# Performance work log

Hardware: AMD Instinct MI355X
Metric: run time of the kernel (lower is better)

Reference implementation:

```python
import jax, jax.numpy as jnp
import numpy as np

L = 2000          # number of residues (sequence length)
FEATURES_L = 2048 # config.features_L pad target
W = 7             # config.window_size
D = 54            # per-residue feature dim after bert_lin
H = 3             # attention heads
HD = D // H       # head dim = 18
CH = 32           # conv hidden channels
KS = (3, 5, 7)    # config.kernels


def setup_inputs() -> dict:
    key = jax.random.key(0)
    ks = jax.random.split(key, 20)
    n = lambda k, s, sc=0.02: jax.random.normal(k, s, jnp.float32) * sc
    return {
        'beft_f': jax.random.normal(ks[0], (L, 1024), jnp.float32),
        'pssm_f': jax.random.normal(ks[1], (L, 20), jnp.float32),
        'hmm_f': jax.random.normal(ks[2], (L, 30), jnp.float32),
        'dssp_f': jax.random.normal(ks[3], (L, 14), jnp.float32),
        'W_bert': n(ks[4], (1024, D)), 'b_bert': jnp.zeros((D,), jnp.float32),
        'ln_g1': jnp.ones((D,), jnp.float32), 'ln_b1': jnp.zeros((D,), jnp.float32),
        'ln_g2': jnp.ones((D,), jnp.float32), 'ln_b2': jnp.zeros((D,), jnp.float32),
        'conv1_w': n(ks[5], (CH, 1, 3, 1), 0.1), 'conv1_b': n(ks[6], (CH,), 0.1),
        'prelu_a': jnp.array(0.25, jnp.float32),
        'conv2_w': n(ks[7], (CH, 1, 5, 1), 0.1), 'conv2_b': n(ks[8], (CH,), 0.1),
        'conv3_w': n(ks[9], (CH, 1, 7, 1), 0.1), 'conv3_b': n(ks[10], (CH,), 0.1),
        'W1': n(ks[11], (972, 256)), 'b1': jnp.zeros((256,), jnp.float32),
        'W2': n(ks[12], (CH * 256, 256)), 'b2': jnp.zeros((256,), jnp.float32),
    }


def _ln(x, g, b, eps=1e-5):
    m = x.mean(-1, keepdims=True)
    v = ((x - m) ** 2).mean(-1, keepdims=True)
    return (x - m) * jax.lax.rsqrt(v + eps) * g + b


def _attn(x, g, b):
    # x: (L, W, D); no qkv projections, no 1/sqrt(d) scaling (as in source)
    qh = x.reshape(x.shape[0], W, H, HD)
    s = jnp.einsum('bqhd,bkhd->bhqk', qh, qh)
    p = jax.nn.softmax(s, axis=-1)
    o = jnp.einsum('bhqk,bkhd->bqhd', p, qh).reshape(x.shape[0], W, D)
    return _ln(o, g, b)


def _conv_branch(x, w, bias, k, act):
    pad = (k - 1) // 2
    c = jax.lax.conv_general_dilated(x, w, (1, 1), ((pad, pad), (0, 0)),
                                     dimension_numbers=('NCHW', 'OIHW', 'NCHW'))
    c = act(c + bias[None, :, None, None])
    c = jax.lax.reduce_window(c, -jnp.inf, jax.lax.max,
                              (1, 1, k, 1), (1, 1, 1, 1), 'VALID')
    return c.reshape(c.shape[0], CH, -1)  # (FEATURES_L, 32, (W-k+1)*2D)


def _forward(beft_f, W_bert, b_bert, ln_g1, ln_b1, ln_g2, ln_b2,
             conv1_w, conv1_b, prelu_a, conv2_w, conv2_b, conv3_w, conv3_b,
             W1, b1, W2, b2):
    f = beft_f @ W_bert + b_bert  # (L, 54)
    # sliding-window gather replicating the source python loop exactly:
    # interior rows i in (W, L-W): window = f[i-4 : i+3]; boundary rows: [f[i], 0...0]
    i = jnp.arange(L)
    j = jnp.arange(W)
    gidx = jnp.clip(i[:, None] - (W // 2 + 1) + j[None, :], 0, L - 1)
    win_int = f[gidx]                                   # (L, 7, 54)
    win_bnd = jnp.zeros((L, W, D), f.dtype).at[:, 0].set(f)
    boundary = (i <= W) | (i + W >= L)
    new_f = jnp.where(boundary[:, None, None], win_bnd, win_int)
    sf = _attn(new_f, ln_g1, ln_b1)
    sf = _attn(sf, ln_g2, ln_b2)
    cat = jnp.concatenate([new_f, sf], axis=2)          # (L, 7, 108)
    x = jnp.pad(cat, ((0, FEATURES_L - L), (0, 0), (0, 0)))[:, None]  # (FL,1,7,108)
    prelu = lambda z: jnp.where(z >= 0, z, prelu_a * z)
    feats = jnp.concatenate([
        _conv_branch(x, conv1_w, conv1_b, KS[0], prelu),
        _conv_branch(x, conv2_w, conv2_b, KS[1], jax.nn.relu),
        _conv_branch(x, conv3_w, conv3_b, KS[2], jax.nn.relu)], axis=2)  # (FL,32,972)
    y = feats[:L] @ W1 + b1                             # (L, 32, 256)
    y = y.reshape(L, CH * 256) @ W2 + b2                # (L, 256)
    return jnp.where(y >= 0, y, 0.01 * y)               # leaky_relu


def reference(beft_f, pssm_f, hmm_f, dssp_f, W_bert, b_bert, ln_g1, ln_b1,
              ln_g2, ln_b2, conv1_w, conv1_b, prelu_a, conv2_w, conv2_b,
              conv3_w, conv3_b, W1, b1, W2, b2):
    # pssm_f / hmm_f / dssp_f are accepted but unused in the source forward
    return _forward(beft_f, W_bert, b_bert, ln_g1, ln_b1, ln_g2, ln_b2,
                    conv1_w, conv1_b, prelu_a, conv2_w, conv2_b,
                    conv3_w, conv3_b, W1, b1, W2, b2)
```

## Files before the change

kernel.cpp:

```cpp
#include <hip/hip_runtime.h>

#define L_RES 2000
#define DF 54
#define WIN 7

typedef short bf16x8 __attribute__((ext_vector_type(8)));
typedef float f32x4 __attribute__((ext_vector_type(4)));
typedef unsigned short ushort8v __attribute__((ext_vector_type(8)));

__device__ __forceinline__ unsigned short f2bf(float f) {
    unsigned int u = __float_as_uint(f);
    unsigned int r = (u + 0x7FFFu + ((u >> 16) & 1u)) >> 16;
    return (unsigned short)r;
}
__device__ __forceinline__ float bf2f(unsigned short h) {
    return __uint_as_float(((unsigned int)h) << 16);
}
__device__ __forceinline__ void gload16(const unsigned short* g, unsigned short* l) {
    __builtin_amdgcn_global_load_lds(
        (const __attribute__((address_space(1))) void*)g,
        (__attribute__((address_space(3))) void*)l, 16, 0, 0);
}

__global__ __launch_bounds__(256) void prep_w(const float* __restrict__ Wb,
                                              unsigned short* __restrict__ B2T,
                                              const float* __restrict__ W1,
                                              unsigned short* __restrict__ P) {
    int bid = blockIdx.x;
    if (bid < 768) {
        int idx = bid * 256 + threadIdx.x;
        int n = idx / 3072, col = idx % 3072;
        int seg = col >> 10, k = col & 1023;
        unsigned short r = 0;
        if (n < DF) {
            float v = Wb[(size_t)k * DF + n];
            unsigned short hi = f2bf(v);
            r = (seg < 2) ? hi : f2bf(v - bf2f(hi));
        }
        B2T[idx] = r;
    } else {
        int idx = (bid - 768) * 256 + threadIdx.x;
        int e = idx & 7, l = (idx >> 3) & 63, g = (idx >> 9) & 31, nb = idx >> 14;
        int ks = g >> 1, kk = g & 1;
        int n = nb * 16 + (l & 15);
        int k = ks * 64 + kk * 32 + (l >> 4) * 8 + e;
        P[idx] = (k < 972) ? f2bf(W1[(size_t)k * 256 + n]) : (unsigned short)0;
    }
}

__global__ __launch_bounds__(256) void bert_mfma(const float* __restrict__ beft,
                                                 const unsigned short* __restrict__ B2T,
                                                 float* __restrict__ bpart) {
    __shared__ unsigned short ldsA[128 * 64];
    __shared__ unsigned short ldsB[64 * 64];
    int t = threadIdx.x, w = t >> 6, lane = t & 63;
    int m0 = blockIdx.x * 128;
    int z = blockIdx.y;
    int koff = z * 768;
    int wr = w >> 1, wc = w & 1;
    int arow = lane & 15, kgrp = lane >> 4;

    int cj[4], aD[4];
    const float* aF[4];
    bool vald[4];
    #pragma unroll
    for (int j = 0; j < 4; ++j) {
        int s = j * 256 + t, r = s >> 3, c = s & 7;
        cj[j] = c;
        aD[j] = r * 64 + ((c ^ (r & 7)) * 8);
        vald[j] = (m0 + r) < L_RES;
        aF[j] = beft + (size_t)(vald[j] ? (m0 + r) : 0) * 1024;
    }
    const unsigned short* bS[2]; int bD[2];
    #pragma unroll
    for (int j = 0; j < 2; ++j) {
        int s = j * 256 + t, r = s >> 3, c = s & 7;
        bS[j] = B2T + koff + (size_t)r * 3072 + c * 8;
        bD[j] = r * 64 + ((c ^ (r & 7)) * 8);
    }
    f32x4 acc[4][2];
    #pragma unroll
    for (int mi = 0; mi < 4; ++mi)
        #pragma unroll
        for (int ni = 0; ni < 2; ++ni) acc[mi][ni] = (f32x4)(0.f);

    f32x4 va0[4], va1[4];
    ushort8v vb[2];
    #pragma unroll
    for (int j = 0; j < 4; ++j) {
        int x = koff + cj[j] * 8;
        int bc = x & 1023;
        va0[j] = *(const f32x4*)(aF[j] + bc);
        va1[j] = *(const f32x4*)(aF[j] + bc + 4);
    }
    #pragma unroll
    for (int j = 0; j < 2; ++j) vb[j] = *(const ushort8v*)(bS[j]);

    for (int ks = 0; ks < 12; ++ks) {
        __syncthreads();
        #pragma unroll
        for (int j = 0; j < 4; ++j) {
            int x = koff + ks * 64 + cj[j] * 8;
            int seg = x >> 10;
            ushort8v v;
            #pragma unroll
            for (int e = 0; e < 8; ++e) {
                float val = (e < 4) ? va0[j][e] : va1[j][e - 4];
                if (!vald[j]) val = 0.f;
                unsigned short hi = f2bf(val);
                v[e] = (seg == 1) ? f2bf(val - bf2f(hi)) : hi;
            }
            *(ushort8v*)&ldsA[aD[j]] = v;
        }
        #pragma unroll
        for (int j = 0; j < 2; ++j) *(ushort8v*)&ldsB[bD[j]] = vb[j];
        __syncthreads();
        if (ks + 1 < 12) {
            #pragma unroll
            for (int j = 0; j < 4; ++j) {
                int x = koff + (ks + 1) * 64 + cj[j] * 8;
                int bc = x & 1023;
                va0[j] = *(const f32x4*)(aF[j] + bc);
                va1[j] = *(const f32x4*)(aF[j] + bc + 4);
            }
            #pragma unroll
            for (int j = 0; j < 2; ++j) vb[j] = *(const ushort8v*)(bS[j] + (ks + 1) * 64);
        }
        #pragma unroll
        for (int kk = 0; kk < 2; ++kk) {
            int chunk = kk * 4 + kgrp;
            bf16x8 af[4], bfr[2];
            #pragma unroll
            for (int mi = 0; mi < 4; ++mi) {
                int rl = wr * 64 + mi * 16 + arow;
                af[mi] = *(const bf16x8*)&ldsA[rl * 64 + ((chunk ^ (rl & 7)) * 8)];
            }
            #pragma unroll
            for (int ni = 0; ni < 2; ++ni) {
                int rl = wc * 32 + ni * 16 + arow;
                bfr[ni] = *(const bf16x8*)&ldsB[rl * 64 + ((chunk ^ (rl & 7)) * 8)];
            }
            #pragma unroll
            for (int mi = 0; mi < 4; ++mi)
                #pragma unroll
                for (int ni = 0; ni < 2; ++ni)
                    acc[mi][ni] = __builtin_amdgcn_mfma_f32_16x16x32_bf16(af[mi], bfr[ni], acc[mi][ni], 0, 0, 0);
        }
    }
    #pragma unroll
    for (int ni = 0; ni < 2; ++ni) {
        int n = wc * 32 + ni * 16 + arow;
        #pragma unroll
        for (int mi = 0; mi < 4; ++mi)
            #pragma unroll
            for (int r = 0; r < 4; ++r) {
                int m = m0 + wr * 64 + mi * 16 + kgrp * 4 + r;
                bpart[((size_t)z * 2048 + m) * 64 + n] = acc[mi][ni][r];
            }
    }
}

__device__ __forceinline__ void attn_layer(const float (*in)[DF], float (*out)[DF],
                                           float (*s)[WIN][WIN],
                                           const float* __restrict__ g,
                                           const float* __restrict__ b,
                                           float* mm, float* vv, int t) {
    for (int idx = t; idx < 3 * WIN * WIN; idx += 64) {
        int h = idx / 49, r = idx % 49, q = r / WIN, k = r % WIN;
        float sum = 0.f;
        #pragma unroll
        for (int d = 0; d < 18; ++d) sum = fmaf(in[q][h * 18 + d], in[k][h * 18 + d], sum);
        s[h][q][k] = sum;
    }
    __syncthreads();
    for (int idx = t; idx < 3 * WIN; idx += 64) {
        int h = idx / WIN, q = idx % WIN;
        float mx = s[h][q][0];
        #pragma unroll
        for (int k = 1; k < WIN; ++k) mx = fmaxf(mx, s[h][q][k]);
        float e[WIN], sum = 0.f;
        #pragma unroll
        for (int k = 0; k < WIN; ++k) { e[k] = expf(s[h][q][k] - mx); sum += e[k]; }
        float inv = 1.f / sum;
        #pragma unroll
        for (int k = 0; k < WIN; ++k) s[h][q][k] = e[k] * inv;
    }
    __syncthreads();
    for (int idx = t; idx < WIN * DF; idx += 64) {
        int q = idx / DF, c = idx % DF, h = c / 18;
        float sum = 0.f;
        #pragma unroll
        for (int k = 0; k < WIN; ++k) sum = fmaf(s[h][q][k], in[k][c], sum);
        out[q][c] = sum;
    }
    __syncthreads();
    for (int q = t; q < WIN; q += 64) {
        float m = 0.f;
        for (int c = 0; c < DF; ++c) m += out[q][c];
        m *= (1.f / DF);
        float v = 0.f;
        for (int c = 0; c < DF; ++c) { float d0 = out[q][c] - m; v = fmaf(d0, d0, v); }
        v *= (1.f / DF);
        mm[q] = m; vv[q] = rsqrtf(v + 1e-5f);
    }
    __syncthreads();
    for (int idx = t; idx < WIN * DF; idx += 64) {
        int q = idx / DF, c = idx % DF;
        out[q][c] = (out[q][c] - mm[q]) * vv[q] * g[c] + b[c];
    }
    __syncthreads();
}

__global__ __launch_bounds__(64) void window_attn(const float* __restrict__ bpart,
                                                  const float* __restrict__ bb,
                                                  const float* __restrict__ g1,
                                                  const float* __restrict__ b1,
                                                  const float* __restrict__ g2,
                                                  const float* __restrict__ b2,
                                                  float* __restrict__ cat) {
    int l = blockIdx.x;
    int t = threadIdx.x;
    __shared__ float w[WIN][DF], o1[WIN][DF], o2[WIN][DF];
    __shared__ float s[3][WIN][WIN];
    __shared__ float mm[WIN], vv[WIN];
    bool boundary = (l <= WIN) || (l + WIN >= L_RES);
    for (int idx = t; idx < WIN * DF; idx += 64) {
        int j = idx / DF, d = idx % DF;
        float v = 0.f;
        if (!boundary || j == 0) {
            int lsrc = boundary ? l : (l - 4 + j);
            v = bb[d];
            #pragma unroll
            for (int z = 0; z < 4; ++z) v += bpart[((size_t)z * 2048 + lsrc) * 64 + d];
        }
        w[j][d] = v;
    }
    __syncthreads();
    attn_layer(w, o1, s, g1, b1, mm, vv, t);
    attn_layer(o1, o2, s, g2, b2, mm, vv, t);
    for (int idx = t; idx < WIN * DF; idx += 64) {
        int j = idx / DF, d = idx % DF;
        cat[(size_t)l * 756 + j * 108 + d] = w[j][d];
        cat[(size_t)l * 756 + j * 108 + DF + d] = o2[j][d];
    }
}

__global__ __launch_bounds__(256) void transpose_to_bf16(const float* __restrict__ src,
                                                         unsigned short* __restrict__ dst,
                                                         int M, int N, int Mpad) {
    __shared__ float tile[32][33];
    int m0 = blockIdx.x * 32, n0 = blockIdx.y * 32;
    int c = threadIdx.x % 32, r0 = threadIdx.x / 32;
    #pragma unroll
    for (int rr = 0; rr < 4; ++rr) {
        int r = r0 + rr * 8, m = m0 + r;
        tile[r][c] = (m < M) ? src[(size_t)m * N + n0 + c] : 0.f;
    }
    __syncthreads();
    #pragma unroll
    for (int rr = 0; rr < 4; ++rr) {
        int r = r0 + rr * 8;
        dst[(size_t)(n0 + r) * Mpad + m0 + c] = f2bf(tile[c][r]);
    }
}

__global__ __launch_bounds__(256) void conv_pool(
        const float* __restrict__ cat,
        const float* __restrict__ c1w, const float* __restrict__ c1b,
        const float* __restrict__ pa_p,
        const float* __restrict__ c2w, const float* __restrict__ c2b,
        const float* __restrict__ c3w, const float* __restrict__ c3b,
        unsigned short* __restrict__ Ap, int lbase) {
    int bid = blockIdx.x;
    int b = bid >> 2;
    int ch0 = (bid & 3) * 8;
    int l0 = lbase + b * 4;
    int t = threadIdx.x;
    __shared__ float catl[4 * 756];
    for (int i = t; i < 3024; i += 256) catl[i] = cat[(size_t)l0 * 756 + i];
    __syncthreads();
    float pa = pa_p[0];
    unsigned short* base = Ap + (size_t)b * 128 * 1024;
    int res = t >> 6, dp = t & 63;
    if (dp < 54) {
        int d0 = dp * 2;
        const float* cr = catl + res * 756;
        float colA[WIN], colB[WIN];
        #pragma unroll
        for (int h = 0; h < WIN; ++h) {
            colA[h] = cr[h * 108 + d0];
            colB[h] = cr[h * 108 + d0 + 1];
        }
        for (int c = ch0; c < ch0 + 8; ++c) {
            unsigned short* Arow = base + (size_t)(res * 32 + c) * 1024;
            {
                float w0 = c1w[c * 3], w1 = c1w[c * 3 + 1], w2 = c1w[c * 3 + 2];
                float bb = c1b[c];
                float vA[WIN], vB[WIN];
                #pragma unroll
                for (int h = 0; h < WIN; ++h) {
                    float sA = bb, sB = bb;
                    if (h >= 1) { sA = fmaf(w0, colA[h - 1], sA); sB = fmaf(w0, colB[h - 1], sB); }
                    sA = fmaf(w1, colA[h], sA); sB = fmaf(w1, colB[h], sB);
                    if (h <= 5) { sA = fmaf(w2, colA[h + 1], sA); sB = fmaf(w2, colB[h + 1], sB); }
                    vA[h] = sA >= 0.f ? sA : pa * sA;
                    vB[h] = sB >= 0.f ? sB : pa * sB;
                }
                #pragma unroll
                for (int p = 0; p < 5; ++p) {
                    unsigned int ua = f2bf(fmaxf(fmaxf(vA[p], vA[p + 1]), vA[p + 2]));
                    unsigned int ub = f2bf(fmaxf(fmaxf(vB[p], vB[p + 1]), vB[p + 2]));
                    *(unsigned int*)&Arow[p * 108 + d0] = ua | (ub << 16);
                }
            }
            {
                float wg[5], bb = c2b[c];
                #pragma unroll
                for (int x = 0; x < 5; ++x) wg[x] = c2w[c * 5 + x];
                float vA[WIN], vB[WIN];
                #pragma unroll
                for (int h = 0; h < WIN; ++h) {
                    float sA = bb, sB = bb;
                    #pragma unroll
                    for (int x = 0; x < 5; ++x) {
                        int hh = h + x - 2;
                        if (hh >= 0 && hh <= 6) {
                            sA = fmaf(wg[x], colA[hh], sA);
                            sB = fmaf(wg[x], colB[hh], sB);
                        }
                    }
                    vA[h] = fmaxf(sA, 0.f);
                    vB[h] = fmaxf(sB, 0.f);
                }
                #pragma unroll
                for (int p = 0; p < 3; ++p) {
                    float ma = vA[p], mb = vB[p];
                    #pragma unroll
                    for (int r = 1; r < 5; ++r) { ma = fmaxf(ma, vA[p + r]); mb = fmaxf(mb, vB[p + r]); }
                    unsigned int ua = f2bf(ma), ub = f2bf(mb);
                    *(unsigned int*)&Arow[540 + p * 108 + d0] = ua | (ub << 16);
                }
            }
            {
                float wg[7], bb = c3b[c];
                #pragma unroll
                for (int x = 0; x < 7; ++x) wg[x] = c3w[c * 7 + x];
                float ma = 0.f, mb = 0.f;
                #pragma unroll
                for (int h = 0; h < WIN; ++h) {
                    float sA = bb, sB = bb;
                    #pragma unroll
                    for (int x = 0; x < 7; ++x) {
                        int hh = h + x - 3;
                        if (hh >= 0 && hh <= 6) {
                            sA = fmaf(wg[x], colA[hh], sA);
                            sB = fmaf(wg[x], colB[hh], sB);
                        }
                    }
                    ma = fmaxf(ma, sA);
                    mb = fmaxf(mb, sB);
                }
                unsigned int ua = f2bf(fmaxf(ma, 0.f)), ub = f2bf(fmaxf(mb, 0.f));
                *(unsigned int*)&Arow[864 + d0] = ua | (ub << 16);
            }
        }
    }
    for (int i = t; i < 832; i += 256) {
        int r = i / 26, q = i - r * 26;
        int res2 = r >> 3, c2 = ch0 + (r & 7);
        *(unsigned int*)&base[(size_t)(res2 * 32 + c2) * 1024 + 972 + q * 2] = 0u;
    }
}

__global__ __launch_bounds__(256, 2) void gemm1k(
        const unsigned short* __restrict__ A,
        const unsigned short* __restrict__ P,
        const float* __restrict__ b1v,
        unsigned short* __restrict__ y1, long outRowBase) {
    __shared__ unsigned short ldsA[2][128 * 64];
    int t = threadIdx.x, w = t >> 6, lane = t & 63;
    long m0 = (long)blockIdx.x * 128;
    int arow = lane & 15, kgrp = lane >> 4;
    int ra = lane >> 3, cc = lane & 7;
    int csw = (cc ^ ra) * 8;

    const unsigned short* gA[4]; int rb[4];
    #pragma unroll
    for (int j = 0; j < 4; ++j) {
        int rbase = j * 32 + w * 8;
        gA[j] = A + (size_t)(m0 + rbase + ra) * 1024 + csw;
        rb[j] = rbase * 64;
    }
    f32x4 acc[8][4];
    #pragma unroll
    for (int mi = 0; mi < 8; ++mi)
        #pragma unroll
        for (int ni = 0; ni < 4; ++ni) acc[mi][ni] = (f32x4)(0.f);

    auto loadB = [&](bf16x8 (&dst)[2][4], int ksv) {
        #pragma unroll
        for (int kk = 0; kk < 2; ++kk)
            #pragma unroll
            for (int ni = 0; ni < 4; ++ni)
                dst[kk][ni] = *(const bf16x8*)&P[(((size_t)(w * 4 + ni) * 32 + ksv * 2 + kk) * 64 + lane) * 8];
    };
    auto stage = [&](int ksv, int buf) {
        #pragma unroll
        for (int j = 0; j < 4; ++j) gload16(gA[j] + ksv * 64, &ldsA[buf][rb[j]]);
    };
    auto compute = [&](int buf, bf16x8 (&b)[2][4]) {
        #pragma unroll
        for (int kk = 0; kk < 2; ++kk) {
            int chunk = kk * 4 + kgrp;
            bf16x8 af[8];
            #pragma unroll
            for (int mi = 0; mi < 8; ++mi) {
                int rl = mi * 16 + arow;
                af[mi] = *(const bf16x8*)&ldsA[buf][rl * 64 + ((chunk ^ (rl & 7)) * 8)];
            }
            #pragma unroll
            for (int mi = 0; mi < 8; ++mi)
                #pragma unroll
                for (int ni = 0; ni < 4; ++ni)
                    acc[mi][ni] = __builtin_amdgcn_mfma_f32_16x16x32_bf16(af[mi], b[kk][ni], acc[mi][ni], 0, 0, 0);
        }
    };

    bf16x8 bA[2][4], bB[2][4];
    loadB(bA, 0);
    stage(0, 0);
    __syncthreads();

    #pragma unroll 1
    for (int ks2 = 0; ks2 < 8; ++ks2) {
        int ks = ks2 * 2;
        loadB(bB, ks + 1);
        stage(ks + 1, 1);
        compute(0, bA);
        __syncthreads();
        if (ks + 2 < 16) {
            loadB(bA, ks + 2);
            stage(ks + 2, 0);
        }
        compute(1, bB);
        __syncthreads();
    }
    #pragma unroll
    for (int ni = 0; ni < 4; ++ni) {
        int n = w * 64 + ni * 16 + arow;
        float bv = b1v[n];
        #pragma unroll
        for (int mi = 0; mi < 8; ++mi)
            #pragma unroll
            for (int r = 0; r < 4; ++r) {
                long row = m0 + mi * 16 + kgrp * 4 + r;
                y1[(outRowBase + row) * 256 + n] = f2bf(acc[mi][ni][r] + bv);
            }
    }
}

template<bool EPI_BF16, int ZBITS>
__global__ __launch_bounds__(512) void gemm_tile8(
        const unsigned short* __restrict__ A, long lda,
        const unsigned short* __restrict__ B, long ldb,
        int nk, const float* __restrict__ bias,
        unsigned short* __restrict__ outB, float* __restrict__ outF,
        long outRowBase) {
    __shared__ unsigned short ldsA[128 * 64];
    __shared__ unsigned short ldsB[256 * 64];
    int t = threadIdx.x, w = t >> 6, lane = t & 63;
    int bid = blockIdx.x;
    int z = bid & ((1 << ZBITS) - 1);
    long m0 = (long)(bid >> ZBITS) * 128;
    long koff = (long)z * (long)nk * 64;
    A += koff; B += koff;
    int wr = w >> 2, wc = w & 3;
    int arow = lane & 15, kgrp = lane >> 4;
    int ra = lane >> 3, cc = lane & 7;
    int csw = (cc ^ ra) * 8;

    const unsigned short* gA[2]; const unsigned short* gB[4];
    unsigned short* dA[2]; unsigned short* dB[4];
    #pragma unroll
    for (int j = 0; j < 2; ++j) {
        int rbase = j * 64 + w * 8;
        gA[j] = A + (size_t)(m0 + rbase + ra) * lda + csw;
        dA[j] = &ldsA[rbase * 64];
    }
    #pragma unroll
    for (int j = 0; j < 4; ++j) {
        int rbase = j * 64 + w * 8;
        gB[j] = B + (size_t)(rbase + ra) * ldb + csw;
        dB[j] = &ldsB[rbase * 64];
    }
    f32x4 acc[4][4];
    #pragma unroll
    for (int mi = 0; mi < 4; ++mi)
        #pragma unroll
        for (int ni = 0; ni < 4; ++ni) acc[mi][ni] = (f32x4)(0.f);

    for (int ks = 0; ks < nk; ++ks) {
        #pragma unroll
        for (int j = 0; j < 2; ++j) gload16(gA[j] + ks * 64, dA[j]);
        #pragma unroll
        for (int j = 0; j < 4; ++j) gload16(gB[j] + ks * 64, dB[j]);
        __syncthreads();
        #pragma unroll
        for (int kk = 0; kk < 2; ++kk) {
            int chunk = kk * 4 + kgrp;
            bf16x8 af[4], bfr[4];
            #pragma unroll
            for (int mi = 0; mi < 4; ++mi) {
                int rl = wr * 64 + mi * 16 + arow;
                af[mi] = *(const bf16x8*)&ldsA[rl * 64 + ((chunk ^ (rl & 7)) * 8)];
            }
            #pragma unroll
            for (int ni = 0; ni < 4; ++ni) {
                int rl = wc * 64 + ni * 16 + arow;
                bfr[ni] = *(const bf16x8*)&ldsB[rl * 64 + ((chunk ^ (rl & 7)) * 8)];
            }
            #pragma unroll
            for (int mi = 0; mi < 4; ++mi)
                #pragma unroll
                for (int ni = 0; ni < 4; ++ni)
                    acc[mi][ni] = __builtin_amdgcn_mfma_f32_16x16x32_bf16(af[mi], bfr[ni], acc[mi][ni], 0, 0, 0);
        }
        __syncthreads();
    }
    #pragma unroll
    for (int ni = 0; ni < 4; ++ni) {
        int n = wc * 64 + ni * 16 + arow;
        float bv = EPI_BF16 ? bias[n] : 0.f;
        #pragma unroll
        for (int mi = 0; mi < 4; ++mi)
            #pragma unroll
            for (int r = 0; r < 4; ++r) {
                long m = m0 + wr * 64 + mi * 16 + kgrp * 4 + r;
                if (EPI_BF16)
                    outB[(outRowBase + m) * 256 + n] = f2bf(acc[mi][ni][r] + bv);
                else
                    outF[((long)z * 2048 + m) * 256 + n] = acc[mi][ni][r];
            }
    }
}

__global__ __launch_bounds__(256) void reduce2(const float* __restrict__ part,
                                               const float* __restrict__ b2v,
                                               float* __restrict__ out) {
    int l = blockIdx.x, n = threadIdx.x;
    float sum = b2v[n];
    #pragma unroll
    for (int s = 0; s < 16; ++s) sum += part[((size_t)s * 2048 + l) * 256 + n];
    out[(size_t)l * 256 + n] = sum >= 0.f ? sum : 0.01f * sum;
}

extern "C" void kernel_launch(void* const* d_in, const int* in_sizes, int n_in,
                              void* d_out, int out_size, void* d_ws, size_t ws_size,
                              hipStream_t stream) {
    const float* beft = (const float*)d_in[0];
    const float* Wb  = (const float*)d_in[4];
    const float* bb  = (const float*)d_in[5];
    const float* g1  = (const float*)d_in[6];
    const float* b1  = (const float*)d_in[7];
    const float* g2  = (const float*)d_in[8];
    const float* b2  = (const float*)d_in[9];
    const float* c1w = (const float*)d_in[10];
    const float* c1b = (const float*)d_in[11];
    const float* pa  = (const float*)d_in[12];
    const float* c2w = (const float*)d_in[13];
    const float* c2b = (const float*)d_in[14];
    const float* c3w = (const float*)d_in[15];
    const float* c3b = (const float*)d_in[16];
    const float* W1  = (const float*)d_in[17];
    const float* b1v = (const float*)d_in[18];
    const float* W2  = (const float*)d_in[19];
    const float* b2v = (const float*)d_in[20];
    float* out = (float*)d_out;
    char* ws = (char*)d_ws;

    float*          cat  = (float*)(ws + 524288);
    unsigned short* W1Tp = (unsigned short*)(ws + 8388608);
    unsigned short* W2T  = (unsigned short*)(ws + 8912896);
    unsigned short* y1   = (unsigned short*)(ws + 13107200);
    unsigned short* B2T  = (unsigned short*)(ws + 25690112);
    float*          bpart= (float*)(ws + 46661632);
    unsigned short* Ap   = (unsigned short*)(ws + 46661632);
    float*          part = (float*)(ws + 46661632);

    long avail = (long)ws_size - 46661632L;
    long tpc = avail / (128L * 1024L * 2L);
    if (tpc < 1) tpc = 1;
    if (tpc > 500) tpc = 500;

    prep_w<<<1792, 256, 0, stream>>>(Wb, B2T, W1, W1Tp);
    bert_mfma<<<dim3(16, 4), 256, 0, stream>>>(beft, B2T, bpart);
    window_attn<<<L_RES, 64, 0, stream>>>(bpart, bb, g1, b1, g2, b2, cat);
    transpose_to_bf16<<<dim3(256, 8), 256, 0, stream>>>(W2, W2T, 8192, 256, 8192);

    for (long t0 = 0; t0 < 500; t0 += tpc) {
        long nt = (500 - t0 < tpc) ? (500 - t0) : tpc;
        conv_pool<<<(int)(nt * 4), 256, 0, stream>>>(cat, c1w, c1b, pa, c2w, c2b,
                                                     c3w, c3b, Ap, (int)(t0 * 4));
        gemm1k<<<(int)nt, 256, 0, stream>>>(Ap, W1Tp, b1v, y1, t0 * 128);
    }
    gemm_tile8<false, 4><<<256, 512, 0, stream>>>(
        y1, 8192, W2T, 8192, 8, nullptr, nullptr, part, 0);
    reduce2<<<L_RES, 256, 0, stream>>>(part, b2v, out);
}
```

Before: 149.2 us.

## Fold W1 and W2 into a combined weight and run one big GEMM

Because the two linear layers have no nonlinearity between them, the change precomputes a per-channel combined weight W1·W2_c (a 1024×256 block for each of the 32 channels) with an MFMA GEMM. It also folds b1·W2 into a bias vector. The pooled conv features then go through a single K=32768 GEMM split across 8 K-slices, followed by a reduction, replacing the gemm1k plus gemm_tile8 chain and the chunked loop. This drops the y1 intermediate and one GEMM over activations. In exchange, every call pays for building the combined weights (about 2 GFLOP), and the product is rounded to bf16, which may cost some accuracy.

```diff
diff --git a/kernel.cpp b/kernel.cpp
--- a/kernel.cpp
+++ b/kernel.cpp
@@ -25,7 +25,7 @@
 __global__ __launch_bounds__(256) void prep_w(const float* __restrict__ Wb,
                                               unsigned short* __restrict__ B2T,
                                               const float* __restrict__ W1,
-                                              unsigned short* __restrict__ P) {
+                                              unsigned short* __restrict__ W1b) {
     int bid = blockIdx.x;
     if (bid < 768) {
         int idx = bid * 256 + threadIdx.x;
@@ -40,11 +40,92 @@
         B2T[idx] = r;
     } else {
         int idx = (bid - 768) * 256 + threadIdx.x;
-        int e = idx & 7, l = (idx >> 3) & 63, g = (idx >> 9) & 31, nb = idx >> 14;
-        int ks = g >> 1, kk = g & 1;
-        int n = nb * 16 + (l & 15);
-        int k = ks * 64 + kk * 32 + (l >> 4) * 8 + e;
-        P[idx] = (k < 972) ? f2bf(W1[(size_t)k * 256 + n]) : (unsigned short)0;
+        int m = idx >> 8, j = idx & 255;
+        W1b[idx] = (m < 972) ? f2bf(W1[(size_t)m * 256 + j]) : (unsigned short)0;
+    }
+}
+
+__global__ __launch_bounds__(256) void w2re_build(const float* __restrict__ W2,
+                                                  unsigned short* __restrict__ W2re) {
+    __shared__ float tile[32][33];
+    int c = blockIdx.z;
+    const float* src = W2 + (size_t)c * 65536;
+    unsigned short* dst = W2re + (size_t)c * 65536;
+    int j0 = blockIdx.x * 32, n0 = blockIdx.y * 32;
+    int cc = threadIdx.x % 32, r0 = threadIdx.x / 32;
+    #pragma unroll
+    for (int rr = 0; rr < 4; ++rr) {
+        int r = r0 + rr * 8;
+        tile[r][cc] = src[(size_t)(j0 + r) * 256 + n0 + cc];
+    }
+    __syncthreads();
+    #pragma unroll
+    for (int rr = 0; rr < 4; ++rr) {
+        int r = r0 + rr * 8;
+        dst[(size_t)(n0 + r) * 256 + j0 + cc] = f2bf(tile[cc][r]);
+    }
+}
+
+__global__ __launch_bounds__(256) void bcombp_build(const float* __restrict__ b1,
+                                                    const float* __restrict__ W2,
+                                                    float* __restrict__ bcombp) {
+    int c = blockIdx.x, n = threadIdx.x;
+    float s = 0.f;
+    for (int j = 0; j < 256; ++j)
+        s = fmaf(b1[j], W2[(size_t)(c * 256 + j) * 256 + n], s);
+    bcombp[c * 256 + n] = s;
+}
+
+__global__ __launch_bounds__(256) void gemmW(const unsigned short* __restrict__ W1b,
+                                             const unsigned short* __restrict__ W2re,
+                                             unsigned short* __restrict__ P2) {
+    int t = threadIdx.x, w = t >> 6, lane = t & 63;
+    int bid = blockIdx.x;
+    int c = bid >> 3, mloc = (bid & 7) * 128;
+    int k0g = bid * 128;
+    int arow = lane & 15, kgrp = lane >> 4;
+    f32x4 acc[8][4];
+    #pragma unroll
+    for (int mi = 0; mi < 8; ++mi)
+        #pragma unroll
+        for (int ni = 0; ni < 4; ++ni) acc[mi][ni] = (f32x4)(0.f);
+    #pragma unroll
+    for (int ks = 0; ks < 4; ++ks) {
+        #pragma unroll
+        for (int kk = 0; kk < 2; ++kk) {
+            int kc = ks * 64 + kk * 32 + kgrp * 8;
+            bf16x8 af[8], bfr[4];
+            #pragma unroll
+            for (int mi = 0; mi < 8; ++mi)
+                af[mi] = *(const bf16x8*)&W1b[(size_t)(mloc + mi * 16 + arow) * 256 + kc];
+            #pragma unroll
+            for (int ni = 0; ni < 4; ++ni) {
+                int n = w * 64 + ni * 16 + arow;
+                bfr[ni] = *(const bf16x8*)&W2re[(size_t)(c * 256 + n) * 256 + kc];
+            }
+            #pragma unroll
+            for (int mi = 0; mi < 8; ++mi)
+                #pragma unroll
+                for (int ni = 0; ni < 4; ++ni)
+                    acc[mi][ni] = __builtin_amdgcn_mfma_f32_16x16x32_bf16(af[mi], bfr[ni], acc[mi][ni], 0, 0, 0);
+        }
+    }
+    #pragma unroll
+    for (int ni = 0; ni < 4; ++ni) {
+        int n = w * 64 + ni * 16 + arow;
+        int nb = n >> 4, ar = n & 15;
+        #pragma unroll
+        for (int mi = 0; mi < 8; ++mi) {
+            int k0 = k0g + mi * 16 + kgrp * 4;
+            int zp = k0 >> 11, ksz = (k0 >> 6) & 31, kk2 = (k0 >> 5) & 1;
+            int kg = (k0 >> 3) & 3, e0 = k0 & 7;
+            size_t idx = (((size_t)(zp * 16 + nb) * 64 + ksz * 2 + kk2) * 512)
+                         + (kg * 16 + ar) * 8 + e0;
+            unsigned int lo = (unsigned int)f2bf(acc[mi][ni][0]) | ((unsigned int)f2bf(acc[mi][ni][1]) << 16);
+            unsigned int hi = (unsigned int)f2bf(acc[mi][ni][2]) | ((unsigned int)f2bf(acc[mi][ni][3]) << 16);
+            *(unsigned int*)&P2[idx] = lo;
+            *(unsigned int*)&P2[idx + 2] = hi;
+        }
     }
 }
 
@@ -88,8 +169,7 @@
     ushort8v vb[2];
     #pragma unroll
     for (int j = 0; j < 4; ++j) {
-        int x = koff + cj[j] * 8;
-        int bc = x & 1023;
+        int bc = (koff + cj[j] * 8) & 1023;
         va0[j] = *(const f32x4*)(aF[j] + bc);
         va1[j] = *(const f32x4*)(aF[j] + bc + 4);
     }
@@ -118,8 +198,7 @@
         if (ks + 1 < 12) {
             #pragma unroll
             for (int j = 0; j < 4; ++j) {
-                int x = koff + (ks + 1) * 64 + cj[j] * 8;
-                int bc = x & 1023;
+                int bc = (koff + (ks + 1) * 64 + cj[j] * 8) & 1023;
                 va0[j] = *(const f32x4*)(aF[j] + bc);
                 va1[j] = *(const f32x4*)(aF[j] + bc + 4);
             }
@@ -245,36 +324,17 @@
     }
 }
 
-__global__ __launch_bounds__(256) void transpose_to_bf16(const float* __restrict__ src,
-                                                         unsigned short* __restrict__ dst,
-                                                         int M, int N, int Mpad) {
-    __shared__ float tile[32][33];
-    int m0 = blockIdx.x * 32, n0 = blockIdx.y * 32;
-    int c = threadIdx.x % 32, r0 = threadIdx.x / 32;
-    #pragma unroll
-    for (int rr = 0; rr < 4; ++rr) {
-        int r = r0 + rr * 8, m = m0 + r;
-        tile[r][c] = (m < M) ? src[(size_t)m * N + n0 + c] : 0.f;
-    }
-    __syncthreads();
-    #pragma unroll
-    for (int rr = 0; rr < 4; ++rr) {
-        int r = r0 + rr * 8;
-        dst[(size_t)(n0 + r) * Mpad + m0 + c] = f2bf(tile[c][r]);
-    }
-}
-
 __global__ __launch_bounds__(256) void conv_pool(
         const float* __restrict__ cat,
         const float* __restrict__ c1w, const float* __restrict__ c1b,
         const float* __restrict__ pa_p,
         const float* __restrict__ c2w, const float* __restrict__ c2b,
         const float* __restrict__ c3w, const float* __restrict__ c3b,
-        unsigned short* __restrict__ Ap, int lbase) {
+        unsigned short* __restrict__ Ap) {
     int bid = blockIdx.x;
     int b = bid >> 2;
     int ch0 = (bid & 3) * 8;
-    int l0 = lbase + b * 4;
+    int l0 = b * 4;
     int t = threadIdx.x;
     __shared__ float catl[4 * 756];
     for (int i = t; i < 3024; i += 256) catl[i] = cat[(size_t)l0 * 756 + i];
@@ -372,14 +432,15 @@
     }
 }
 
-__global__ __launch_bounds__(256, 2) void gemm1k(
-        const unsigned short* __restrict__ A,
-        const unsigned short* __restrict__ P,
-        const float* __restrict__ b1v,
-        unsigned short* __restrict__ y1, long outRowBase) {
+__global__ __launch_bounds__(256, 2) void gemmC(const unsigned short* __restrict__ A,
+                                                const unsigned short* __restrict__ P2,
+                                                float* __restrict__ part) {
     __shared__ unsigned short ldsA[2][128 * 64];
     int t = threadIdx.x, w = t >> 6, lane = t & 63;
-    long m0 = (long)blockIdx.x * 128;
+    int bid = blockIdx.x;
+    int nh = bid & 1, z = (bid >> 1) & 7, mt = bid >> 4;
+    long m0 = (long)mt * 128;
+    long kbase = (long)z * 4096;
     int arow = lane & 15, kgrp = lane >> 4;
     int ra = lane >> 3, cc = lane & 7;
     int csw = (cc ^ ra) * 8;
@@ -388,170 +449,75 @@
     #pragma unroll
     for (int j = 0; j < 4; ++j) {
         int rbase = j * 32 + w * 8;
-        gA[j] = A + (size_t)(m0 + rbase + ra) * 1024 + csw;
+        long row = m0 + rbase + ra;
+        if (row >= L_RES) row = 0;
+        gA[j] = A + row * 32768 + kbase + csw;
         rb[j] = rbase * 64;
     }
-    f32x4 acc[8][4];
+    f32x4 acc[8][2];
     #pragma unroll
     for (int mi = 0; mi < 8; ++mi)
         #pragma unroll
-        for (int ni = 0; ni < 4; ++ni) acc[mi][ni] = (f32x4)(0.f);
-
-    auto loadB = [&](bf16x8 (&dst)[2][4], int ksv) {
-        #pragma unroll
-        for (int kk = 0; kk < 2; ++kk)
-            #pragma unroll
-            for (int ni = 0; ni < 4; ++ni)
-                dst[kk][ni] = *(const bf16x8*)&P[(((size_t)(w * 4 + ni) * 32 + ksv * 2 + kk) * 64 + lane) * 8];
-    };
-    auto stage = [&](int ksv, int buf) {
-        #pragma unroll
-        for (int j = 0; j < 4; ++j) gload16(gA[j] + ksv * 64, &ldsA[buf][rb[j]]);
-    };
-    auto compute = [&](int buf, bf16x8 (&b)[2][4]) {
+        for (int ni = 0; ni < 2; ++ni) acc[mi][ni] = (f32x4)(0.f);
+
+    #pragma unroll
+    for (int j = 0; j < 4; ++j) gload16(gA[j], &ldsA[0][rb[j]]);
+    __syncthreads();
+
+    #pragma unroll 1
+    for (int ks = 0; ks < 64; ++ks) {
+        int cur = ks & 1;
+        if (ks + 1 < 64) {
+            #pragma unroll
+            for (int j = 0; j < 4; ++j) gload16(gA[j] + (ks + 1) * 64, &ldsA[cur ^ 1][rb[j]]);
+        }
+        int zp = z * 2 + (ks >> 5), ksz = ks & 31;
         #pragma unroll
         for (int kk = 0; kk < 2; ++kk) {
+            bf16x8 af[8], bfr[2];
+            #pragma unroll
+            for (int ni = 0; ni < 2; ++ni) {
+                int nbG = nh * 8 + w * 2 + ni;
+                bfr[ni] = *(const bf16x8*)&P2[(((size_t)(zp * 16 + nbG) * 64 + ksz * 2 + kk) * 512) + lane * 8];
+            }
             int chunk = kk * 4 + kgrp;
-            bf16x8 af[8];
             #pragma unroll
             for (int mi = 0; mi < 8; ++mi) {
                 int rl = mi * 16 + arow;
-                af[mi] = *(const bf16x8*)&ldsA[buf][rl * 64 + ((chunk ^ (rl & 7)) * 8)];
+                af[mi] = *(const bf16x8*)&ldsA[cur][rl * 64 + ((chunk ^ (rl & 7)) * 8)];
             }
             #pragma unroll
             for (int mi = 0; mi < 8; ++mi)
                 #pragma unroll
-                for (int ni = 0; ni < 4; ++ni)
-                    acc[mi][ni] = __builtin_amdgcn_mfma_f32_16x16x32_bf16(af[mi], b[kk][ni], acc[mi][ni], 0, 0, 0);
-        }
-    };
-
-    bf16x8 bA[2][4], bB[2][4];
-    loadB(bA, 0);
-    stage(0, 0);
-    __syncthreads();
-
-    #pragma unroll 1
-    for (int ks2 = 0; ks2 < 8; ++ks2) {
-        int ks = ks2 * 2;
-        loadB(bB, ks + 1);
-        stage(ks + 1, 1);
-        compute(0, bA);
+                for (int ni = 0; ni < 2; ++ni)
+                    acc[mi][ni] = __builtin_amdgcn_mfma_f32_16x16x32_bf16(af[mi], bfr[ni], acc[mi][ni], 0, 0, 0);
+        }
         __syncthreads();
-        if (ks + 2 < 16) {
-            loadB(bA, ks + 2);
-            stage(ks + 2, 0);
-        }
-        compute(1, bB);
-        __syncthreads();
-    }
-    #pragma unroll
-    for (int ni = 0; ni < 4; ++ni) {
-        int n = w * 64 + ni * 16 + arow;
-        float bv = b1v[n];
+    }
+    #pragma unroll
+    for (int ni = 0; ni < 2; ++ni) {
+        int n = nh * 128 + w * 32 + ni * 16 + arow;
         #pragma unroll
         for (int mi = 0; mi < 8; ++mi)
             #pragma unroll
             for (int r = 0; r < 4; ++r) {
                 long row = m0 + mi * 16 + kgrp * 4 + r;
-                y1[(outRowBase + row) * 256 + n] = f2bf(acc[mi][ni][r] + bv);
-            }
-    }
-}
-
-template<bool EPI_BF16, int ZBITS>
-__global__ __launch_bounds__(512) void gemm_tile8(
-        const unsigned short* __restrict__ A, long lda,
-        const unsigned short* __restrict__ B, long ldb,
-        int nk, const float* __restrict__ bias,
-        unsigned short* __restrict__ outB, float* __restrict__ outF,
-        long outRowBase) {
-    __shared__ unsigned short ldsA[128 * 64];
-    __shared__ unsigned short ldsB[256 * 64];
-    int t = threadIdx.x, w = t >> 6, lane = t & 63;
-    int bid = blockIdx.x;
-    int z = bid & ((1 << ZBITS) - 1);
-    long m0 = (long)(bid >> ZBITS) * 128;
-    long koff = (long)z * (long)nk * 64;
-    A += koff; B += koff;
-    int wr = w >> 2, wc = w & 3;
-    int arow = lane & 15, kgrp = lane >> 4;
-    int ra = lane >> 3, cc = lane & 7;
-    int csw = (cc ^ ra) * 8;
-
-    const unsigned short* gA[2]; const unsigned short* gB[4];
-    unsigned short* dA[2]; unsigned short* dB[4];
-    #pragma unroll
-    for (int j = 0; j < 2; ++j) {
-        int rbase = j * 64 + w * 8;
-        gA[j] = A + (size_t)(m0 + rbase + ra) * lda + csw;
-        dA[j] = &ldsA[rbase * 64];
-    }
-    #pragma unroll
-    for (int j = 0; j < 4; ++j) {
-        int rbase = j * 64 + w * 8;
-        gB[j] = B + (size_t)(rbase + ra) * ldb + csw;
-        dB[j] = &ldsB[rbase * 64];
-    }
-    f32x4 acc[4][4];
-    #pragma unroll
-    for (int mi = 0; mi < 4; ++mi)
-        #pragma unroll
-        for (int ni = 0; ni < 4; ++ni) acc[mi][ni] = (f32x4)(0.f);
-
-    for (int ks = 0; ks < nk; ++ks) {
-        #pragma unroll
-        for (int j = 0; j < 2; ++j) gload16(gA[j] + ks * 64, dA[j]);
-        #pragma unroll
-        for (int j = 0; j < 4; ++j) gload16(gB[j] + ks * 64, dB[j]);
-        __syncthreads();
-        #pragma unroll
-        for (int kk = 0; kk < 2; ++kk) {
-            int chunk = kk * 4 + kgrp;
-            bf16x8 af[4], bfr[4];
-            #pragma unroll
-            for (int mi = 0; mi < 4; ++mi) {
-                int rl = wr * 64 + mi * 16 + arow;
-                af[mi] = *(const bf16x8*)&ldsA[rl * 64 + ((chunk ^ (rl & 7)) * 8)];
-            }
-            #pragma unroll
-            for (int ni = 0; ni < 4; ++ni) {
-                int rl = wc * 64 + ni * 16 + arow;
-                bfr[ni] = *(const bf16x8*)&ldsB[rl * 64 + ((chunk ^ (rl & 7)) * 8)];
-            }
-            #pragma unroll
-            for (int mi = 0; mi < 4; ++mi)
-                #pragma unroll
-                for (int ni = 0; ni < 4; ++ni)
-                    acc[mi][ni] = __builtin_amdgcn_mfma_f32_16x16x32_bf16(af[mi], bfr[ni], acc[mi][ni], 0, 0, 0);
-        }
-        __syncthreads();
-    }
-    #pragma unroll
-    for (int ni = 0; ni < 4; ++ni) {
-        int n = wc * 64 + ni * 16 + arow;
-        float bv = EPI_BF16 ? bias[n] : 0.f;
-        #pragma unroll
-        for (int mi = 0; mi < 4; ++mi)
-            #pragma unroll
-            for (int r = 0; r < 4; ++r) {
-                long m = m0 + wr * 64 + mi * 16 + kgrp * 4 + r;
-                if (EPI_BF16)
-                    outB[(outRowBase + m) * 256 + n] = f2bf(acc[mi][ni][r] + bv);
-                else
-                    outF[((long)z * 2048 + m) * 256 + n] = acc[mi][ni][r];
-            }
-    }
-}
-
-__global__ __launch_bounds__(256) void reduce2(const float* __restrict__ part,
+                part[((size_t)z * 2048 + row) * 256 + n] = acc[mi][ni][r];
+            }
+    }
+}
+
+__global__ __launch_bounds__(256) void reduceC(const float* __restrict__ part,
+                                               const float* __restrict__ bcombp,
                                                const float* __restrict__ b2v,
                                                float* __restrict__ out) {
     int l = blockIdx.x, n = threadIdx.x;
-    float sum = b2v[n];
-    #pragma unroll
-    for (int s = 0; s < 16; ++s) sum += part[((size_t)s * 2048 + l) * 256 + n];
-    out[(size_t)l * 256 + n] = sum >= 0.f ? sum : 0.01f * sum;
+    float s = b2v[n];
+    #pragma unroll
+    for (int c = 0; c < 32; ++c) s += bcombp[c * 256 + n];
+    #pragma unroll
+    for (int z = 0; z < 8; ++z) s += part[((size_t)z * 2048 + l) * 256 + n];
+    out[(size_t)l * 256 + n] = s >= 0.f ? s : 0.01f * s;
 }
 
 extern "C" void kernel_launch(void* const* d_in, const int* in_sizes, int n_in,
@@ -578,32 +544,23 @@
     float* out = (float*)d_out;
     char* ws = (char*)d_ws;
 
-    float*          cat  = (float*)(ws + 524288);
-    unsigned short* W1Tp = (unsigned short*)(ws + 8388608);
-    unsigned short* W2T  = (unsigned short*)(ws + 8912896);
-    unsigned short* y1   = (unsigned short*)(ws + 13107200);
-    unsigned short* B2T  = (unsigned short*)(ws + 25690112);
-    float*          bpart= (float*)(ws + 46661632);
-    unsigned short* Ap   = (unsigned short*)(ws + 46661632);
-    float*          part = (float*)(ws + 46661632);
-
-    long avail = (long)ws_size - 46661632L;
-    long tpc = avail / (128L * 1024L * 2L);
-    if (tpc < 1) tpc = 1;
-    if (tpc > 500) tpc = 500;
-
-    prep_w<<<1792, 256, 0, stream>>>(Wb, B2T, W1, W1Tp);
+    float*          bpart = (float*)(ws + 0);
+    float*          cat   = (float*)(ws + 2097152);
+    unsigned short* B2T   = (unsigned short*)(ws + 8388608);
+    unsigned short* W1b   = (unsigned short*)(ws + 8781824);
+    unsigned short* W2re  = (unsigned short*)(ws + 9306112);
+    float*          part  = (float*)(ws + 0);
+    unsigned short* P2    = (unsigned short*)(ws + 16777216);
+    float*          bcombp= (float*)(ws + 33554432);
+    unsigned short* Apool = (unsigned short*)(ws + 33587200);
+
+    prep_w<<<1792, 256, 0, stream>>>(Wb, B2T, W1, W1b);
+    w2re_build<<<dim3(8, 8, 32), 256, 0, stream>>>(W2, W2re);
+    bcombp_build<<<32, 256, 0, stream>>>(b1v, W2, bcombp);
     bert_mfma<<<dim3(16, 4), 256, 0, stream>>>(beft, B2T, bpart);
     window_attn<<<L_RES, 64, 0, stream>>>(bpart, bb, g1, b1, g2, b2, cat);
-    transpose_to_bf16<<<dim3(256, 8), 256, 0, stream>>>(W2, W2T, 8192, 256, 8192);
-
-    for (long t0 = 0; t0 < 500; t0 += tpc) {
-        long nt = (500 - t0 < tpc) ? (500 - t0) : tpc;
-        conv_pool<<<(int)(nt * 4), 256, 0, stream>>>(cat, c1w, c1b, pa, c2w, c2b,
-                                                     c3w, c3b, Ap, (int)(t0 * 4));
-        gemm1k<<<(int)nt, 256, 0, stream>>>(Ap, W1Tp, b1v, y1, t0 * 128);
-    }
-    gemm_tile8<false, 4><<<256, 512, 0, stream>>>(
-        y1, 8192, W2T, 8192, 8, nullptr, nullptr, part, 0);
-    reduce2<<<L_RES, 256, 0, stream>>>(part, b2v, out);
-}
+    gemmW<<<256, 256, 0, stream>>>(W1b, W2re, P2);
+    conv_pool<<<2000, 256, 0, stream>>>(cat, c1w, c1b, pa, c2w, c2b, c3w, c3b, Apool);
+    gemmC<<<256, 256, 0, stream>>>(Apool, P2, part);
+    reduceC<<<L_RES, 256, 0, stream>>>(part, bcombp, b2v, out);
+}
```

Measured after the change: 192.4 us. 28.9% more time.
